# Kernel tuning notes

Measured on AMD Instinct MI355X. Metric: run time of the kernel, lower is better.

The kernel has to match this reference:

```python
import jax, jax.numpy as jnp
import numpy as np

B, D = 1024, 768


def setup_inputs() -> dict:
    key = jax.random.key(0)
    k1, k2 = jax.random.split(key)
    image_features = jax.random.normal(k1, (B, D), dtype=jnp.float32)
    # plant a few exact duplicate rows so the label-propagation path is nontrivial
    image_features = image_features.at[17].set(image_features[3])
    image_features = image_features.at[512].set(image_features[3])
    image_features = image_features.at[900].set(image_features[128])
    text_features = jax.random.normal(k2, (B, D), dtype=jnp.float32)
    logit_scale = jnp.float32(14.285714)  # exp(log(1/0.07)), standard CLIP init
    return {"image_features": image_features, "text_features": text_features, "logit_scale": logit_scale}


def reference(image_features, text_features, logit_scale):
    # logits_per_image: [B, B]
    logits = logit_scale * (image_features @ text_features.T)
    # Duplicate detection: the original O(B^2) python loop assigns to row j the
    # index of the FIRST row i (i <= j) whose features exactly equal row j.
    # eq[i, j] = rows i and j are elementwise identical
    eq = jnp.all(image_features[:, None, :] == image_features[None, :, :], axis=-1)  # [B, B] bool
    labels = jnp.argmax(eq, axis=0)  # first matching index per row (diag guarantees a hit)
    # cross-entropy with integer labels, mean over batch
    logp = jax.nn.log_softmax(logits, axis=1)
    loss = -jnp.mean(jnp.take_along_axis(logp, labels[:, None], axis=1))
    return loss
```

## Files before the change

kernel.cpp:

```cpp
#include <hip/hip_runtime.h>
#include <stdint.h>

#define BATCH 1024
#define DIM 768

typedef unsigned long long u64;
typedef __attribute__((ext_vector_type(8))) short short8;
typedef __attribute__((ext_vector_type(4))) float f32x4;

#define WS_ACC  8192
#define WS_PMAX 12288
#define WS_PSUM 28672
#define WS_TXTB 49152

__device__ __forceinline__ unsigned short to_bf16(float x) {
    unsigned int u = __float_as_uint(x);
    return (unsigned short)((u + 0x7FFFu + ((u >> 16) & 1u)) >> 16);
}

__global__ __launch_bounds__(256) void prep_kernel(
        const float* __restrict__ img, const float* __restrict__ txt,
        u64* __restrict__ hashes, float* __restrict__ acc, int* __restrict__ counter,
        unsigned short* __restrict__ txtB) {
    if (blockIdx.x == 0 && threadIdx.x == 0) { *acc = 0.0f; *counter = 0; }
    const int wave = threadIdx.x >> 6;
    const int lane = threadIdx.x & 63;

    for (int i = wave; i < 6; i += 4) {
        const int G  = blockIdx.x * 6 + i;
        const int tt = G / 24;
        const int g  = G - tt * 24;
        const int col = tt * 16 + (lane & 15);
        const int k0  = g * 32 + (lane >> 4) * 8;
        const float4 va = *(const float4*)(txt + (size_t)col * DIM + k0);
        const float4 vb = *(const float4*)(txt + (size_t)col * DIM + k0 + 4);
        short8 hv = {(short)to_bf16(va.x), (short)to_bf16(va.y),
                     (short)to_bf16(va.z), (short)to_bf16(va.w),
                     (short)to_bf16(vb.x), (short)to_bf16(vb.y),
                     (short)to_bf16(vb.z), (short)to_bf16(vb.w)};
        *(short8*)(txtB + (size_t)(g * 64 + tt) * 512 + lane * 8) = hv;
    }

    const int row = blockIdx.x * 4 + wave;
    const float4* rp = (const float4*)(img + (size_t)row * DIM);
    u64 h = 0;
#pragma unroll
    for (int c = 0; c < 3; ++c) {
        float4 v = rp[c * 64 + lane];
        int p = c * 256 + lane * 4;
        h += ((u64)__float_as_uint(v.x) + 0x9E3779B97F4A7C15ULL) * (u64)(2 * p + 1);
        h += ((u64)__float_as_uint(v.y) + 0x9E3779B97F4A7C15ULL) * (u64)(2 * p + 3);
        h += ((u64)__float_as_uint(v.z) + 0x9E3779B97F4A7C15ULL) * (u64)(2 * p + 5);
        h += ((u64)__float_as_uint(v.w) + 0x9E3779B97F4A7C15ULL) * (u64)(2 * p + 7);
    }
#pragma unroll
    for (int m = 32; m; m >>= 1) h += __shfl_xor(h, m, 64);
    if (lane == 0) hashes[row] = h;
}

__global__ __launch_bounds__(1024) void gemm_kernel(
        const float* __restrict__ img, const float* __restrict__ scale_p,
        const unsigned short* __restrict__ txtB,
        float* __restrict__ pmax, float* __restrict__ psum) {
    __shared__ unsigned short Ahi[16 * DIM];
    __shared__ float logitsS[16 * 260];

    const int tid  = threadIdx.x;
    const int wave = tid >> 6;
    const int lane = tid & 63;
    const int quad = lane >> 4;
    const int l15  = lane & 15;
    const int r0    = (blockIdx.x >> 2) * 16;
    const int chunk = blockIdx.x & 3;

    {
        const float* ir = img + (size_t)(r0 + wave) * DIM;
#pragma unroll
        for (int j = 0; j < 12; ++j) {
            const int k = lane + j * 64;
            Ahi[((k >> 3) * 16 + wave) * 8 + (k & 7)] = to_bf16(ir[k]);
        }
    }
    __syncthreads();

    const int t = chunk * 16 + wave;
    const int foff = quad * 128 + l15 * 8;
    f32x4 acc = {0.f, 0.f, 0.f, 0.f};
#pragma unroll
    for (int kk = 0; kk < 24; ++kk) {
        const short8 a = *(const short8*)&Ahi[kk * 512 + foff];
        const short8 b = *(const short8*)(txtB + (size_t)(kk * 64 + t) * 512 + foff);
        acc = __builtin_amdgcn_mfma_f32_16x16x32_bf16(a, b, acc, 0, 0, 0);
    }

    const float scale = scale_p[0];
#pragma unroll
    for (int r = 0; r < 4; ++r)
        logitsS[(quad * 4 + r) * 260 + wave * 16 + l15] = scale * acc[r];
    __syncthreads();

    {
        const float4 f = *(const float4*)&logitsS[wave * 260 + lane * 4];
        float mx = fmaxf(fmaxf(f.x, f.y), fmaxf(f.z, f.w));
#pragma unroll
        for (int s = 32; s; s >>= 1) mx = fmaxf(mx, __shfl_xor(mx, s, 64));
        float sum = __expf(f.x - mx) + __expf(f.y - mx) +
                    __expf(f.z - mx) + __expf(f.w - mx);
#pragma unroll
        for (int s = 32; s; s >>= 1) sum += __shfl_xor(sum, s, 64);
        if (lane == 0) {
            pmax[(r0 + wave) * 4 + chunk] = mx;
            psum[(r0 + wave) * 4 + chunk] = sum;
        }
    }
}

__global__ __launch_bounds__(1024) void final_kernel(
        const float* __restrict__ img, const float* __restrict__ txt,
        const float* __restrict__ scale_p, const u64* __restrict__ hashes,
        const float* __restrict__ pmax, const float* __restrict__ psum,
        float* __restrict__ acc, int* __restrict__ counter,
        float* __restrict__ out) {
    const int tid  = threadIdx.x;
    const int wave = tid >> 6;
    const int lane = tid & 63;
    const int j = blockIdx.x * 16 + wave;

    const u64 hj = hashes[j];
    int cand = BATCH;
    for (int i = lane; i < j; i += 64)
        if (hashes[i] == hj) { cand = i; break; }
    int label = j;
    for (;;) {
        int mm = cand;
#pragma unroll
        for (int s = 32; s; s >>= 1) mm = min(mm, __shfl_xor(mm, s, 64));
        if (mm >= j) break;
        const float4* rpm = (const float4*)(img + (size_t)mm * DIM);
        const float4* rpj = (const float4*)(img + (size_t)j * DIM);
        bool eq = true;
#pragma unroll
        for (int c = 0; c < 3; ++c) {
            float4 vm = rpm[c * 64 + lane];
            float4 vj = rpj[c * 64 + lane];
            eq = eq && (vm.x == vj.x) && (vm.y == vj.y) &&
                 (vm.z == vj.z) && (vm.w == vj.w);
        }
        if (__all(eq)) { label = mm; break; }
        if (cand == mm) {
            cand = BATCH;
            for (int i = mm + 64; i < j; i += 64)
                if (hashes[i] == hj) { cand = i; break; }
        }
    }

    const float4* aj = (const float4*)(img + (size_t)j * DIM);
    const float4* bl = (const float4*)(txt + (size_t)label * DIM);
    float s = 0.0f;
#pragma unroll
    for (int c = 0; c < 3; ++c) {
        const float4 va = aj[c * 64 + lane];
        const float4 vb = bl[c * 64 + lane];
        s += va.x * vb.x + va.y * vb.y + va.z * vb.z + va.w * vb.w;
    }
#pragma unroll
    for (int m = 32; m; m >>= 1) s += __shfl_xor(s, m, 64);

    if (lane == 0) {
        const float lval = scale_p[0] * s;
        const float m0 = pmax[j * 4 + 0], m1 = pmax[j * 4 + 1];
        const float m2 = pmax[j * 4 + 2], m3 = pmax[j * 4 + 3];
        const float gmax = fmaxf(fmaxf(m0, m1), fmaxf(m2, m3));
        const float ss = psum[j * 4 + 0] * __expf(m0 - gmax)
                       + psum[j * 4 + 1] * __expf(m1 - gmax)
                       + psum[j * 4 + 2] * __expf(m2 - gmax)
                       + psum[j * 4 + 3] * __expf(m3 - gmax);
        const float lse = gmax + __logf(ss);
        atomicAdd(acc, lse - lval);
    }
    __syncthreads();

    if (tid == 0) {
        __threadfence();
        const int old = atomicAdd(counter, 1);
        if (old == (int)gridDim.x - 1) {
            __threadfence();
            out[0] = (*(volatile float*)acc) * (1.0f / BATCH);
        }
    }
}

extern "C" void kernel_launch(void* const* d_in, const int* in_sizes, int n_in,
                              void* d_out, int out_size, void* d_ws, size_t ws_size,
                              hipStream_t stream) {
    const float* img   = (const float*)d_in[0];
    const float* txt   = (const float*)d_in[1];
    const float* scale = (const float*)d_in[2];
    float* out = (float*)d_out;
    char* ws = (char*)d_ws;

    u64*   hashes  = (u64*)ws;
    float* acc     = (float*)(ws + WS_ACC);
    int*   counter = (int*)(ws + WS_ACC + 4);
    float* pmax    = (float*)(ws + WS_PMAX);
    float* psum    = (float*)(ws + WS_PSUM);
    unsigned short* txtB = (unsigned short*)(ws + WS_TXTB);

    prep_kernel<<<256, 256, 0, stream>>>(img, txt, hashes, acc, counter, txtB);
    gemm_kernel<<<256, 1024, 0, stream>>>(img, scale, txtB, pmax, psum);
    final_kernel<<<64, 1024, 0, stream>>>(img, txt, scale, hashes, pmax, psum,
                                          acc, counter, out);
}
```

Measured before the change: 86.19 us.

## Fuse final loss kernel into GEMM via per-row-group last-block counters

Merges the final label/log-sum-exp kernel into the GEMM kernel. Each row group's four chunk blocks bump a per-group atomic counter, and the last one to finish does the label search and loss accumulation for those 16 rows. This removes one kernel launch and the gap between kernels. In exchange it adds atomic release/acquire traffic and leaves the final work on only one of the four blocks per group.

New measurement: 286.6 us. 3.33x slower.

```diff
diff --git a/kernel.cpp b/kernel.cpp
--- a/kernel.cpp
+++ b/kernel.cpp
@@ -9,6 +9,7 @@
 typedef __attribute__((ext_vector_type(4))) float f32x4;
 
 #define WS_ACC  8192
+#define WS_RGC  8200
 #define WS_PMAX 12288
 #define WS_PSUM 28672
 #define WS_TXTB 49152
@@ -21,8 +22,11 @@
 __global__ __launch_bounds__(256) void prep_kernel(
         const float* __restrict__ img, const float* __restrict__ txt,
         u64* __restrict__ hashes, float* __restrict__ acc, int* __restrict__ counter,
-        unsigned short* __restrict__ txtB) {
-    if (blockIdx.x == 0 && threadIdx.x == 0) { *acc = 0.0f; *counter = 0; }
+        int* __restrict__ rgc, unsigned short* __restrict__ txtB) {
+    if (blockIdx.x == 0) {
+        if (threadIdx.x < 64) rgc[threadIdx.x] = 0;
+        else if (threadIdx.x == 64) { *acc = 0.0f; *counter = 0; }
+    }
     const int wave = threadIdx.x >> 6;
     const int lane = threadIdx.x & 63;
 
@@ -58,20 +62,25 @@
     if (lane == 0) hashes[row] = h;
 }
 
-__global__ __launch_bounds__(1024) void gemm_kernel(
-        const float* __restrict__ img, const float* __restrict__ scale_p,
+__global__ __launch_bounds__(1024) void gemm_final_kernel(
+        const float* __restrict__ img, const float* __restrict__ txt,
+        const float* __restrict__ scale_p, const u64* __restrict__ hashes,
         const unsigned short* __restrict__ txtB,
-        float* __restrict__ pmax, float* __restrict__ psum) {
+        float* __restrict__ pmax, float* __restrict__ psum,
+        float* __restrict__ acc, int* __restrict__ counter, int* __restrict__ rgc,
+        float* __restrict__ out) {
     __shared__ unsigned short Ahi[16 * DIM];
     __shared__ float logitsS[16 * 260];
+    __shared__ int is_last_s;
 
     const int tid  = threadIdx.x;
     const int wave = tid >> 6;
     const int lane = tid & 63;
     const int quad = lane >> 4;
     const int l15  = lane & 15;
-    const int r0    = (blockIdx.x >> 2) * 16;
+    const int rg    = blockIdx.x >> 2;
     const int chunk = blockIdx.x & 3;
+    const int r0    = rg * 16;
 
     {
         const float* ir = img + (size_t)(r0 + wave) * DIM;
@@ -85,18 +94,18 @@
 
     const int t = chunk * 16 + wave;
     const int foff = quad * 128 + l15 * 8;
-    f32x4 acc = {0.f, 0.f, 0.f, 0.f};
+    f32x4 a4 = {0.f, 0.f, 0.f, 0.f};
 #pragma unroll
     for (int kk = 0; kk < 24; ++kk) {
         const short8 a = *(const short8*)&Ahi[kk * 512 + foff];
         const short8 b = *(const short8*)(txtB + (size_t)(kk * 64 + t) * 512 + foff);
-        acc = __builtin_amdgcn_mfma_f32_16x16x32_bf16(a, b, acc, 0, 0, 0);
+        a4 = __builtin_amdgcn_mfma_f32_16x16x32_bf16(a, b, a4, 0, 0, 0);
     }
 
     const float scale = scale_p[0];
 #pragma unroll
     for (int r = 0; r < 4; ++r)
-        logitsS[(quad * 4 + r) * 260 + wave * 16 + l15] = scale * acc[r];
+        logitsS[(quad * 4 + r) * 260 + wave * 16 + l15] = scale * a4[r];
     __syncthreads();
 
     {
@@ -109,22 +118,25 @@
 #pragma unroll
         for (int s = 32; s; s >>= 1) sum += __shfl_xor(sum, s, 64);
         if (lane == 0) {
-            pmax[(r0 + wave) * 4 + chunk] = mx;
-            psum[(r0 + wave) * 4 + chunk] = sum;
-        }
-    }
-}
-
-__global__ __launch_bounds__(1024) void final_kernel(
-        const float* __restrict__ img, const float* __restrict__ txt,
-        const float* __restrict__ scale_p, const u64* __restrict__ hashes,
-        const float* __restrict__ pmax, const float* __restrict__ psum,
-        float* __restrict__ acc, int* __restrict__ counter,
-        float* __restrict__ out) {
-    const int tid  = threadIdx.x;
-    const int wave = tid >> 6;
-    const int lane = tid & 63;
-    const int j = blockIdx.x * 16 + wave;
+            __hip_atomic_store(&pmax[(r0 + wave) * 4 + chunk], mx,
+                               __ATOMIC_RELEASE, __HIP_MEMORY_SCOPE_AGENT);
+            __hip_atomic_store(&psum[(r0 + wave) * 4 + chunk], sum,
+                               __ATOMIC_RELEASE, __HIP_MEMORY_SCOPE_AGENT);
+        }
+    }
+    __syncthreads();
+
+    if (tid == 0) {
+        __threadfence();
+        const int old = __hip_atomic_fetch_add(&rgc[rg], 1, __ATOMIC_ACQ_REL,
+                                               __HIP_MEMORY_SCOPE_AGENT);
+        is_last_s = (old == 3);
+    }
+    __syncthreads();
+    if (!is_last_s) return;
+    __threadfence();
+
+    const int j = r0 + wave;
 
     const u64 hj = hashes[j];
     int cand = BATCH;
@@ -168,24 +180,29 @@
 
     if (lane == 0) {
         const float lval = scale_p[0] * s;
-        const float m0 = pmax[j * 4 + 0], m1 = pmax[j * 4 + 1];
-        const float m2 = pmax[j * 4 + 2], m3 = pmax[j * 4 + 3];
+        const float m0 = __hip_atomic_load(&pmax[j*4+0], __ATOMIC_ACQUIRE, __HIP_MEMORY_SCOPE_AGENT);
+        const float m1 = __hip_atomic_load(&pmax[j*4+1], __ATOMIC_ACQUIRE, __HIP_MEMORY_SCOPE_AGENT);
+        const float m2 = __hip_atomic_load(&pmax[j*4+2], __ATOMIC_ACQUIRE, __HIP_MEMORY_SCOPE_AGENT);
+        const float m3 = __hip_atomic_load(&pmax[j*4+3], __ATOMIC_ACQUIRE, __HIP_MEMORY_SCOPE_AGENT);
+        const float s0 = __hip_atomic_load(&psum[j*4+0], __ATOMIC_ACQUIRE, __HIP_MEMORY_SCOPE_AGENT);
+        const float s1 = __hip_atomic_load(&psum[j*4+1], __ATOMIC_ACQUIRE, __HIP_MEMORY_SCOPE_AGENT);
+        const float s2 = __hip_atomic_load(&psum[j*4+2], __ATOMIC_ACQUIRE, __HIP_MEMORY_SCOPE_AGENT);
+        const float s3 = __hip_atomic_load(&psum[j*4+3], __ATOMIC_ACQUIRE, __HIP_MEMORY_SCOPE_AGENT);
         const float gmax = fmaxf(fmaxf(m0, m1), fmaxf(m2, m3));
-        const float ss = psum[j * 4 + 0] * __expf(m0 - gmax)
-                       + psum[j * 4 + 1] * __expf(m1 - gmax)
-                       + psum[j * 4 + 2] * __expf(m2 - gmax)
-                       + psum[j * 4 + 3] * __expf(m3 - gmax);
-        const float lse = gmax + __logf(ss);
-        atomicAdd(acc, lse - lval);
+        const float ss = s0 * __expf(m0 - gmax) + s1 * __expf(m1 - gmax)
+                       + s2 * __expf(m2 - gmax) + s3 * __expf(m3 - gmax);
+        atomicAdd(acc, gmax + __logf(ss) - lval);
     }
     __syncthreads();
 
     if (tid == 0) {
         __threadfence();
-        const int old = atomicAdd(counter, 1);
-        if (old == (int)gridDim.x - 1) {
+        const int old = __hip_atomic_fetch_add(counter, 1, __ATOMIC_ACQ_REL,
+                                               __HIP_MEMORY_SCOPE_AGENT);
+        if (old == 63) {
             __threadfence();
-            out[0] = (*(volatile float*)acc) * (1.0f / BATCH);
+            out[0] = __hip_atomic_load(acc, __ATOMIC_ACQUIRE,
+                                       __HIP_MEMORY_SCOPE_AGENT) * (1.0f / BATCH);
         }
     }
 }
@@ -202,12 +219,12 @@
     u64*   hashes  = (u64*)ws;
     float* acc     = (float*)(ws + WS_ACC);
     int*   counter = (int*)(ws + WS_ACC + 4);
+    int*   rgc     = (int*)(ws + WS_RGC);
     float* pmax    = (float*)(ws + WS_PMAX);
     float* psum    = (float*)(ws + WS_PSUM);
     unsigned short* txtB = (unsigned short*)(ws + WS_TXTB);
 
-    prep_kernel<<<256, 256, 0, stream>>>(img, txt, hashes, acc, counter, txtB);
-    gemm_kernel<<<256, 1024, 0, stream>>>(img, scale, txtB, pmax, psum);
-    final_kernel<<<64, 1024, 0, stream>>>(img, txt, scale, hashes, pmax, psum,
-                                          acc, counter, out);
-}
+    prep_kernel<<<256, 256, 0, stream>>>(img, txt, hashes, acc, counter, rgc, txtB);
+    gemm_final_kernel<<<256, 1024, 0, stream>>>(img, txt, scale, hashes, txtB,
+                                                pmax, psum, acc, counter, rgc, out);
+}
```
